# Kernel tuning notes

Hardware: AMD Instinct MI355X
Metric: run time of the kernel (lower is better)

The kernel has to match this reference:

```python
import jax, jax.numpy as jnp
import numpy as np


def setup_inputs() -> dict:
    key = jax.random.key(0)
    k1, k2, k3 = jax.random.split(key, 3)
    B, M, K, C = 4, 64, 32, 256
    ch, red = K * K, 2
    x = jax.random.normal(k1, (B, M, K, C), dtype=jnp.float32)
    # 1x1 conv weights (bias=False): squeeze spatial dims -> plain matrices
    W1 = jax.random.normal(k2, (ch // red, ch), dtype=jnp.float32) * 0.02
    W2 = jax.random.normal(k3, (ch, ch // red), dtype=jnp.float32) * 0.02
    return {"x": x, "W1": W1, "W2": W2}


def reference(x, W1, W2):
    B, M, K, C = x.shape
    # ---- Pearson correlation (Bessel-corrected), matches self.pearson ----
    cen = x - x.mean(axis=-1, keepdims=True)                       # [B,M,K,C]
    cov = jnp.einsum('bmic,bmjc->bmij', cen, cen) / (C - 1)         # [B,M,K,K]
    std = jnp.sqrt(jnp.sum(cen * cen, axis=-1) / (C - 1))           # [B,M,K]
    adj = cov / (std[..., :, None] * std[..., None, :])             # [B,M,K,K]
    # ---- attention scores: concat([x_i, pos*x_j]) then avgpool over 2C ----
    # pos = 1 where x_i == x_j elementwise else 2
    xi = x[:, :, :, None, :]                                        # [B,M,K,1,C]
    xj = x[:, :, None, :, :]                                        # [B,M,1,K,C]
    pos = jnp.where(xi == xj, jnp.float32(1.0), jnp.float32(2.0))   # [B,M,K,K,C]
    # AdaptiveAvgPool2d((None,1)) over the 2C concat = mean of both halves
    pooled = 0.5 * (x.mean(-1)[:, :, :, None] + jnp.mean(pos * xj, axis=-1))  # [B,M,K,K]
    # conv input channel index is i*K+j -> reshape to [B, K*K, M]
    p = pooled.transpose(0, 2, 3, 1).reshape(B, K * K, M)
    h = jax.nn.gelu(jnp.einsum('oc,bcm->bom', W1, p), approximate=False)
    e = jax.nn.sigmoid(jnp.einsum('oc,bcm->bom', W2, h))            # [B,K*K,M]
    e = e.transpose(0, 2, 1).reshape(B, M, K, K)
    # ---- masked softmax + aggregation ----
    NEG = jnp.float32(-9e15)
    attention = jax.nn.softmax(jnp.where(adj > 0, e, NEG), axis=-1)
    out = jnp.einsum('bmij,bmjc->bmic', attention, x)               # [B,M,K,C]
    return out, adj
```

## Files before the change

kernel.cpp:

```cpp
#include <hip/hip_runtime.h>
#include <math.h>

#define KK 32
#define CC 256

__global__ __launch_bounds__(256) void prep_kernel(
    const float* __restrict__ x, const float* __restrict__ W1,
    float* __restrict__ mean_ws, float* __restrict__ A_ws,
    float* __restrict__ adj_out)
{
    __shared__ float xs[KK][258];
    __shared__ float part8[256];
    __shared__ float meanv[KK];
    __shared__ float covm[KK][KK + 1];
    __shared__ float stdv[KK];
    __shared__ float rowlds[1056];

    const int t = threadIdx.x;

    if (blockIdx.x >= 256) {
        const int o = blockIdx.x - 256;
        if (t < 64) {
            const float* wr = W1 + (size_t)o * 1024;
            #pragma unroll
            for (int u = 0; u < 4; ++u) {
                const int e = t * 16 + u * 4;
                const float4 v = *(const float4*)(wr + e);
                const int f = (e >> 5) * 33 + (e & 31);
                rowlds[f] = v.x; rowlds[f + 1] = v.y;
                rowlds[f + 2] = v.z; rowlds[f + 3] = v.w;
            }
        }
        __syncthreads();
        if (t < 32) {
            float rs = 0.f, cs = 0.f;
            #pragma unroll
            for (int j = 0; j < 32; ++j) rs += rowlds[t * 33 + j];
            #pragma unroll
            for (int i = 0; i < 32; ++i) cs += rowlds[i * 33 + t];
            const float diag = rowlds[t * 34];
            A_ws[o * 32 + t] = 0.5f * rs + cs - 0.5f * diag;
        }
        return;
    }

    const int bm = blockIdx.x;
    const int b  = bm >> 6, m = bm & 63;
    const float* xp = x + (size_t)bm * (KK * CC);

    #pragma unroll
    for (int s = 0; s < 8; ++s) {
        const int e = s * 1024 + t * 4;
        const float4 v = *(const float4*)(xp + e);
        const int i = e >> 8, col = e & 255;
        xs[i][col] = v.x; xs[i][col + 1] = v.y;
        xs[i][col + 2] = v.z; xs[i][col + 3] = v.w;
    }
    __syncthreads();

    {
        const int i = t >> 3, part = t & 7;
        float s = 0.f;
        const int c0 = part * 32;
        #pragma unroll
        for (int c = 0; c < 32; ++c) s += xs[i][c0 + c];
        part8[t] = s;
    }
    __syncthreads();
    if (t < KK) {
        float s = 0.f;
        #pragma unroll
        for (int k = 0; k < 8; ++k) s += part8[t * 8 + k];
        meanv[t] = s * (1.0f / CC);
        mean_ws[(size_t)(b * 32 + t) * 64 + m] = meanv[t];
    }
    __syncthreads();

    {
        const int r = t >> 3, c0 = (t & 7) * 32;
        const float mv = meanv[r];
        #pragma unroll
        for (int c = 0; c < 32; ++c) xs[r][c0 + c] -= mv;
    }
    __syncthreads();

    if (t < 136) {
        int rem = t, r = 0;
        while (rem >= 16 - r) { rem -= 16 - r; ++r; }
        const int ti = r, tj = r + rem;
        const int i0 = 2 * ti, i1 = i0 + 1, j0 = 2 * tj, j1 = j0 + 1;
        float c00 = 0.f, c01 = 0.f, c10 = 0.f, c11 = 0.f;
        for (int c = 0; c < CC; c += 2) {
            const float2 a0 = *(const float2*)&xs[i0][c];
            const float2 a1 = *(const float2*)&xs[i1][c];
            const float2 b0 = *(const float2*)&xs[j0][c];
            const float2 b1 = *(const float2*)&xs[j1][c];
            c00 += a0.x * b0.x; c00 += a0.y * b0.y;
            c01 += a0.x * b1.x; c01 += a0.y * b1.y;
            c10 += a1.x * b0.x; c10 += a1.y * b0.y;
            c11 += a1.x * b1.x; c11 += a1.y * b1.y;
        }
        c00 *= (1.0f / (CC - 1)); c01 *= (1.0f / (CC - 1));
        c10 *= (1.0f / (CC - 1)); c11 *= (1.0f / (CC - 1));
        covm[i0][j0] = c00; covm[i0][j1] = c01;
        covm[i1][j0] = c10; covm[i1][j1] = c11;
        covm[j0][i0] = c00; covm[j1][i0] = c01;
        covm[j0][i1] = c10; covm[j1][i1] = c11;
    }
    __syncthreads();
    if (t < KK) stdv[t] = sqrtf(covm[t][t]);
    __syncthreads();
    #pragma unroll
    for (int k = 0; k < 4; ++k) {
        const int pair = t + k * 256;
        const int i = pair >> 5, j = pair & 31;
        adj_out[(size_t)bm * 1024 + pair] = covm[i][j] / (stdv[i] * stdv[j]);
    }
}

__global__ __launch_bounds__(64) void mlp1_kernel(
    const float* __restrict__ A_ws, const float* __restrict__ mean_ws,
    float* __restrict__ h_ws)
{
    const int m = threadIdx.x;
    const int b = blockIdx.y;
    const int ob = blockIdx.x * 4;
    float mr[32];
    #pragma unroll
    for (int k = 0; k < 32; ++k) mr[k] = mean_ws[(size_t)(b * 32 + k) * 64 + m];
    #pragma unroll
    for (int q = 0; q < 4; ++q) {
        const float* Ar = A_ws + (size_t)(ob + q) * 32;
        float a = 0.f;
        #pragma unroll
        for (int k = 0; k < 32; ++k) a += Ar[k] * mr[k];
        const float g = 0.5f * a * (1.0f + erff(a * 0.70710678118654752f));
        h_ws[(size_t)(b * 512 + ob + q) * 64 + m] = g;
    }
}

__global__ __launch_bounds__(256) void mlp2_kernel(
    const float* __restrict__ W2, const float* __restrict__ h_ws,
    float* __restrict__ e_ws)
{
    __shared__ float W2s[16][512];
    const int m  = threadIdx.x;
    const int ow = threadIdx.y;
    const int b  = blockIdx.y;
    const int ob = blockIdx.x * 16;

    {
        const int t = ow * 64 + m;
        const float* src = W2 + (size_t)ob * 512;
        #pragma unroll
        for (int u = 0; u < 8; ++u) {
            const int e4 = t + u * 256;
            const float4 v = *(const float4*)(src + e4 * 4);
            *(float4*)&W2s[e4 >> 7][(e4 & 127) * 4] = v;
        }
    }
    __syncthreads();

    const float* hb = h_ws + (size_t)b * 512 * 64 + m;
    float acc[4] = {0.f, 0.f, 0.f, 0.f};
    const int ol = ow * 4;

    for (int c = 0; c < 512; c += 4) {
        const float hv0 = hb[(size_t)(c + 0) * 64];
        const float hv1 = hb[(size_t)(c + 1) * 64];
        const float hv2 = hb[(size_t)(c + 2) * 64];
        const float hv3 = hb[(size_t)(c + 3) * 64];
        #pragma unroll
        for (int q = 0; q < 4; ++q) {
            const float4 w = *(const float4*)&W2s[ol + q][c];
            acc[q] += w.x * hv0;
            acc[q] += w.y * hv1;
            acc[q] += w.z * hv2;
            acc[q] += w.w * hv3;
        }
    }
    #pragma unroll
    for (int q = 0; q < 4; ++q) {
        const int o = ob + ol + q;
        e_ws[(size_t)(b * 1024 + o) * 64 + m] = 1.0f / (1.0f + expf(-acc[q]));
    }
}

__global__ __launch_bounds__(256) void softmax_out_kernel(
    const float* __restrict__ x, const float* __restrict__ e_ws,
    const float* __restrict__ adj, float* __restrict__ out)
{
    __shared__ float xs[KK][260];
    __shared__ float att[KK][KK + 1];
    const int bm = blockIdx.x;
    const int b  = bm >> 6, m = bm & 63;
    const int t  = threadIdx.x;
    const float* xp = x + (size_t)bm * (KK * CC);

    #pragma unroll
    for (int s = 0; s < 8; ++s) {
        const int e = s * 1024 + t * 4;
        const float4 v = *(const float4*)(xp + e);
        *(float4*)&xs[e >> 8][e & 255] = v;
    }
    #pragma unroll
    for (int k = 0; k < 4; ++k) {
        const int pair = t + k * 256;
        const int i = pair >> 5, j = pair & 31;
        const float a  = adj[(size_t)bm * 1024 + pair];
        const float ev = e_ws[(size_t)(b * 1024 + pair) * 64 + m];
        att[i][j] = (a > 0.f) ? ev : -INFINITY;
    }
    __syncthreads();
    if (t < KK) {
        float mx = -INFINITY;
        #pragma unroll
        for (int j = 0; j < KK; ++j) mx = fmaxf(mx, att[t][j]);
        float s = 0.f;
        #pragma unroll
        for (int j = 0; j < KK; ++j) {
            const float v = expf(att[t][j] - mx);
            att[t][j] = v;
            s += v;
        }
        const float inv = 1.0f / s;
        #pragma unroll
        for (int j = 0; j < KK; ++j) att[t][j] *= inv;
    }
    __syncthreads();

    const int c8 = t & 31, iq = t >> 5;
    const int i0 = iq * 4;
    const int cA = 4 * c8, cB = 128 + 4 * c8;
    float4 accA[4], accB[4];
    #pragma unroll
    for (int r = 0; r < 4; ++r) {
        accA[r] = make_float4(0.f, 0.f, 0.f, 0.f);
        accB[r] = make_float4(0.f, 0.f, 0.f, 0.f);
    }
    for (int j = 0; j < KK; ++j) {
        const float4 xa = *(const float4*)&xs[j][cA];
        const float4 xb = *(const float4*)&xs[j][cB];
        #pragma unroll
        for (int r = 0; r < 4; ++r) {
            const float av = att[i0 + r][j];
            accA[r].x += av * xa.x; accA[r].y += av * xa.y;
            accA[r].z += av * xa.z; accA[r].w += av * xa.w;
            accB[r].x += av * xb.x; accB[r].y += av * xb.y;
            accB[r].z += av * xb.z; accB[r].w += av * xb.w;
        }
    }
    float* op = out + (size_t)bm * (KK * CC);
    #pragma unroll
    for (int r = 0; r < 4; ++r) {
        *(float4*)(op + (size_t)(i0 + r) * CC + cA) = accA[r];
        *(float4*)(op + (size_t)(i0 + r) * CC + cB) = accB[r];
    }
}

extern "C" void kernel_launch(void* const* d_in, const int* in_sizes, int n_in,
                              void* d_out, int out_size, void* d_ws, size_t ws_size,
                              hipStream_t stream) {
    const float* x  = (const float*)d_in[0];
    const float* W1 = (const float*)d_in[1];
    const float* W2 = (const float*)d_in[2];
    float* out     = (float*)d_out;
    float* adj_out = out + (size_t)4 * 64 * 32 * 256;

    float* mean_ws = (float*)d_ws;
    float* A_ws    = mean_ws + 8192;
    float* h_ws    = A_ws + 16384;
    float* e_ws    = h_ws + 131072;

    prep_kernel<<<768, 256, 0, stream>>>(x, W1, mean_ws, A_ws, adj_out);
    mlp1_kernel<<<dim3(128, 4), 64, 0, stream>>>(A_ws, mean_ws, h_ws);
    mlp2_kernel<<<dim3(64, 4), dim3(64, 4), 0, stream>>>(W2, h_ws, e_ws);
    softmax_out_kernel<<<256, 256, 0, stream>>>(x, e_ws, adj_out, out);
}
```

Before: 102.1 us.

## Fuse MLP stages into one kernel and transpose e workspace layout

Merges the GELU first-layer kernel and the sigmoid second-layer kernel into one kernel. Each block recomputes the hidden activations for its batch in shared memory, in two halves, rather than writing them to global memory and reading them back. The e workspace is stored as [b,m,pair] so the softmax kernel can read it with one coalesced float4 load per thread instead of strided scalar loads. The cost is redundant recomputation of the first layer in all 64 blocks per batch, plus larger shared memory use that may limit occupancy.

```diff
diff --git a/kernel.cpp b/kernel.cpp
--- a/kernel.cpp
+++ b/kernel.cpp
@@ -4,9 +4,9 @@
 #define KK 32
 #define CC 256
 
-__global__ __launch_bounds__(256) void prep_kernel(
+__global__ __launch_bounds__(256) void stats_a_kernel(
     const float* __restrict__ x, const float* __restrict__ W1,
-    float* __restrict__ mean_ws, float* __restrict__ A_ws,
+    float* __restrict__ A_ws, float* __restrict__ mean_ws,
     float* __restrict__ adj_out)
 {
     __shared__ float xs[KK][258];
@@ -14,11 +14,11 @@
     __shared__ float meanv[KK];
     __shared__ float covm[KK][KK + 1];
     __shared__ float stdv[KK];
-    __shared__ float rowlds[1056];
 
     const int t = threadIdx.x;
 
     if (blockIdx.x >= 256) {
+        float* rowlds = &xs[0][0];
         const int o = blockIdx.x - 256;
         if (t < 64) {
             const float* wr = W1 + (size_t)o * 1024;
@@ -38,8 +38,7 @@
             for (int j = 0; j < 32; ++j) rs += rowlds[t * 33 + j];
             #pragma unroll
             for (int i = 0; i < 32; ++i) cs += rowlds[i * 33 + t];
-            const float diag = rowlds[t * 34];
-            A_ws[o * 32 + t] = 0.5f * rs + cs - 0.5f * diag;
+            A_ws[o * 32 + t] = 0.5f * rs + cs - 0.5f * rowlds[t * 34];
         }
         return;
     }
@@ -57,7 +56,6 @@
         xs[i][col + 2] = v.z; xs[i][col + 3] = v.w;
     }
     __syncthreads();
-
     {
         const int i = t >> 3, part = t & 7;
         float s = 0.f;
@@ -75,7 +73,6 @@
         mean_ws[(size_t)(b * 32 + t) * 64 + m] = meanv[t];
     }
     __syncthreads();
-
     {
         const int r = t >> 3, c0 = (t & 7) * 32;
         const float mv = meanv[r];
@@ -83,7 +80,6 @@
         for (int c = 0; c < 32; ++c) xs[r][c0 + c] -= mv;
     }
     __syncthreads();
-
     if (t < 136) {
         int rem = t, r = 0;
         while (rem >= 16 - r) { rem -= 16 - r; ++r; }
@@ -118,72 +114,78 @@
     }
 }
 
-__global__ __launch_bounds__(64) void mlp1_kernel(
+__global__ __launch_bounds__(256) void mlp_fused_kernel(
     const float* __restrict__ A_ws, const float* __restrict__ mean_ws,
-    float* __restrict__ h_ws)
+    const float* __restrict__ W2, float* __restrict__ e_ws)
 {
-    const int m = threadIdx.x;
-    const int b = blockIdx.y;
-    const int ob = blockIdx.x * 4;
-    float mr[32];
-    #pragma unroll
-    for (int k = 0; k < 32; ++k) mr[k] = mean_ws[(size_t)(b * 32 + k) * 64 + m];
-    #pragma unroll
-    for (int q = 0; q < 4; ++q) {
-        const float* Ar = A_ws + (size_t)(ob + q) * 32;
-        float a = 0.f;
-        #pragma unroll
-        for (int k = 0; k < 32; ++k) a += Ar[k] * mr[k];
-        const float g = 0.5f * a * (1.0f + erff(a * 0.70710678118654752f));
-        h_ws[(size_t)(b * 512 + ob + q) * 64 + m] = g;
-    }
-}
-
-__global__ __launch_bounds__(256) void mlp2_kernel(
-    const float* __restrict__ W2, const float* __restrict__ h_ws,
-    float* __restrict__ e_ws)
-{
-    __shared__ float W2s[16][512];
-    const int m  = threadIdx.x;
-    const int ow = threadIdx.y;
+    __shared__ float hsh[256][64];
+    __shared__ float W2s[16][256];
+    __shared__ float mu[32][64];
+
+    const int t  = threadIdx.x;
+    const int m  = t & 63, ow = t >> 6;
     const int b  = blockIdx.y;
     const int ob = blockIdx.x * 16;
-
-    {
-        const int t = ow * 64 + m;
-        const float* src = W2 + (size_t)ob * 512;
-        #pragma unroll
-        for (int u = 0; u < 8; ++u) {
-            const int e4 = t + u * 256;
-            const float4 v = *(const float4*)(src + e4 * 4);
-            *(float4*)&W2s[e4 >> 7][(e4 & 127) * 4] = v;
-        }
-    }
-    __syncthreads();
-
-    const float* hb = h_ws + (size_t)b * 512 * 64 + m;
+    const int ol = ow * 4;
+
+    #pragma unroll
+    for (int u = 0; u < 8; ++u) {
+        const int e = t + u * 256;
+        mu[e >> 6][e & 63] = mean_ws[(size_t)(b * 32) * 64 + e];
+    }
+    __syncthreads();
+
+    float mr[32];
+    #pragma unroll
+    for (int k = 0; k < 32; ++k) mr[k] = mu[k][m];
+
     float acc[4] = {0.f, 0.f, 0.f, 0.f};
-    const int ol = ow * 4;
-
-    for (int c = 0; c < 512; c += 4) {
-        const float hv0 = hb[(size_t)(c + 0) * 64];
-        const float hv1 = hb[(size_t)(c + 1) * 64];
-        const float hv2 = hb[(size_t)(c + 2) * 64];
-        const float hv3 = hb[(size_t)(c + 3) * 64];
-        #pragma unroll
-        for (int q = 0; q < 4; ++q) {
-            const float4 w = *(const float4*)&W2s[ol + q][c];
-            acc[q] += w.x * hv0;
-            acc[q] += w.y * hv1;
-            acc[q] += w.z * hv2;
-            acc[q] += w.w * hv3;
-        }
-    }
-    #pragma unroll
-    for (int q = 0; q < 4; ++q) {
-        const int o = ob + ol + q;
-        e_ws[(size_t)(b * 1024 + o) * 64 + m] = 1.0f / (1.0f + expf(-acc[q]));
-    }
+
+    #pragma unroll
+    for (int half = 0; half < 2; ++half) {
+        for (int i = 0; i < 64; ++i) {
+            const int cl = ow * 64 + i;
+            const int c  = half * 256 + cl;
+            const float* Ar = A_ws + (size_t)c * 32;
+            float a = 0.f;
+            #pragma unroll
+            for (int k = 0; k < 32; ++k) a += Ar[k] * mr[k];
+            hsh[cl][m] = 0.5f * a * (1.0f + erff(a * 0.70710678118654752f));
+        }
+        {
+            const float* src = W2 + (size_t)ob * 512 + half * 256;
+            #pragma unroll
+            for (int u = 0; u < 4; ++u) {
+                const int e4 = t + u * 256;
+                const int row = e4 >> 6, c4 = (e4 & 63) * 4;
+                *(float4*)&W2s[row][c4] =
+                    *(const float4*)(src + (size_t)row * 512 + c4);
+            }
+        }
+        __syncthreads();
+        for (int cl = 0; cl < 256; cl += 4) {
+            const float hv0 = hsh[cl][m];
+            const float hv1 = hsh[cl + 1][m];
+            const float hv2 = hsh[cl + 2][m];
+            const float hv3 = hsh[cl + 3][m];
+            #pragma unroll
+            for (int q = 0; q < 4; ++q) {
+                const float4 w = *(const float4*)&W2s[ol + q][cl];
+                acc[q] += w.x * hv0;
+                acc[q] += w.y * hv1;
+                acc[q] += w.z * hv2;
+                acc[q] += w.w * hv3;
+            }
+        }
+        __syncthreads();
+    }
+
+    float4 sv;
+    sv.x = 1.0f / (1.0f + expf(-acc[0]));
+    sv.y = 1.0f / (1.0f + expf(-acc[1]));
+    sv.z = 1.0f / (1.0f + expf(-acc[2]));
+    sv.w = 1.0f / (1.0f + expf(-acc[3]));
+    *(float4*)&e_ws[(size_t)(b * 64 + m) * 1024 + ob + ol] = sv;
 }
 
 __global__ __launch_bounds__(256) void softmax_out_kernel(
@@ -203,13 +205,15 @@
         const float4 v = *(const float4*)(xp + e);
         *(float4*)&xs[e >> 8][e & 255] = v;
     }
-    #pragma unroll
-    for (int k = 0; k < 4; ++k) {
-        const int pair = t + k * 256;
-        const int i = pair >> 5, j = pair & 31;
-        const float a  = adj[(size_t)bm * 1024 + pair];
-        const float ev = e_ws[(size_t)(b * 1024 + pair) * 64 + m];
-        att[i][j] = (a > 0.f) ? ev : -INFINITY;
+    {
+        const int p0 = 4 * t;
+        const float4 ev4 = *(const float4*)&e_ws[(size_t)(b * 64 + m) * 1024 + p0];
+        const float4 aj4 = *(const float4*)&adj[(size_t)bm * 1024 + p0];
+        const int i = p0 >> 5, j0 = p0 & 31;
+        att[i][j0]     = (aj4.x > 0.f) ? ev4.x : -INFINITY;
+        att[i][j0 + 1] = (aj4.y > 0.f) ? ev4.y : -INFINITY;
+        att[i][j0 + 2] = (aj4.z > 0.f) ? ev4.z : -INFINITY;
+        att[i][j0 + 3] = (aj4.w > 0.f) ? ev4.w : -INFINITY;
     }
     __syncthreads();
     if (t < KK) {
@@ -267,13 +271,11 @@
     float* out     = (float*)d_out;
     float* adj_out = out + (size_t)4 * 64 * 32 * 256;
 
-    float* mean_ws = (float*)d_ws;
-    float* A_ws    = mean_ws + 8192;
-    float* h_ws    = A_ws + 16384;
-    float* e_ws    = h_ws + 131072;
-
-    prep_kernel<<<768, 256, 0, stream>>>(x, W1, mean_ws, A_ws, adj_out);
-    mlp1_kernel<<<dim3(128, 4), 64, 0, stream>>>(A_ws, mean_ws, h_ws);
-    mlp2_kernel<<<dim3(64, 4), dim3(64, 4), 0, stream>>>(W2, h_ws, e_ws);
+    float* A_ws    = (float*)d_ws;
+    float* mean_ws = A_ws + 16384;
+    float* e_ws    = mean_ws + 8192;
+
+    stats_a_kernel<<<768, 256, 0, stream>>>(x, W1, A_ws, mean_ws, adj_out);
+    mlp_fused_kernel<<<dim3(64, 4), 256, 0, stream>>>(A_ws, mean_ws, W2, e_ws);
     softmax_out_kernel<<<256, 256, 0, stream>>>(x, e_ws, adj_out, out);
 }
```

Result: slower. 143.0 us (+40.0%).
